# Kernel optimization log

Hardware: AMD Instinct MI355X
Metric: run time of the kernel (lower is better)

## Reference

```python
import jax, jax.numpy as jnp
import numpy as np

N, E, D, H = 50000, 600000, 128, 128
SLOPE = 0.01  # default negative_slope of F.leaky_relu / nn.LeakyReLU


def leaky(x):
    return jnp.where(x >= 0, x, SLOPE * x)


def gcn_conv(x, src, dst, W, b, n):
    """PyG GCNConv: x' = D^{-1/2}(A+I)D^{-1/2} (x W) + b, symmetric norm with self-loops."""
    h = x @ W  # [n, out]
    ones = jnp.ones(src.shape[0], h.dtype)
    deg = jax.ops.segment_sum(ones, dst, num_segments=n) + 1.0  # +1 for self-loop
    dinv = jax.lax.rsqrt(deg)  # deg >= 1 always
    norm = dinv[src] * dinv[dst]  # per-edge coefficient
    msg = h[src] * norm[:, None]  # gather + scale: [E, out]
    agg = jax.ops.segment_sum(msg, dst, num_segments=n)  # scatter-add
    agg = agg + h * (dinv * dinv)[:, None]  # self-loop term
    return agg + b


def setup_inputs() -> dict:
    key = jax.random.key(0)
    ks = jax.random.split(key, 16)
    kaiming = lambda k, fi, fo: jax.random.normal(k, (fi, fo), jnp.float32) * np.sqrt(2.0 / fi)
    return {
        "x": jax.random.normal(ks[0], (N, D), jnp.float32),
        "edge_index": jax.random.randint(ks[1], (2, E), 0, N, jnp.int64 if jax.config.jax_enable_x64 else jnp.int32),
        "gen_data": jax.random.normal(ks[2], (N, H), jnp.float32),
        "Wc1": kaiming(ks[3], D, H), "bc1": jnp.zeros((H,), jnp.float32),
        "Wc2": kaiming(ks[4], H, H), "bc2": jnp.zeros((H,), jnp.float32),
        "Wm1": kaiming(ks[5], H, H), "bm1": jnp.zeros((H,), jnp.float32),
        "Wm2": kaiming(ks[6], H, H), "bm2": jnp.zeros((H,), jnp.float32),
        "Wp1": kaiming(ks[7], H, H), "bp1": jnp.zeros((H,), jnp.float32),
        "Wp2": kaiming(ks[8], H, H), "bp2": jnp.zeros((H,), jnp.float32),
    }


def reference(x, edge_index, gen_data, Wc1, bc1, Wc2, bc2, Wm1, bm1, Wm2, bm2, Wp1, bp1, Wp2, bp2):
    src, dst = edge_index[0], edge_index[1]
    lambd = 0.5
    # GraphEncoder4Link
    h = leaky(gcn_conv(x, src, dst, Wc1, bc1, N))
    h = leaky(gcn_conv(h, src, dst, Wc2, bc2, N) + h)
    h = leaky((leaky(h @ Wm1 + bm1) @ Wm2 + bm2) + h)
    # lambd interpolation with gen_data
    out = lambd * h + (1.0 - lambd) * gen_data
    # proj MLP
    out = leaky(leaky(out @ Wp1 + bp1) @ Wp2 + bp2)
    return out
```

## Files before the change

### kernel.cpp

```cpp
#include <hip/hip_runtime.h>
#include <cstdint>
#include <cstddef>

#define HH 128
#define SLOPE 0.01f

typedef __attribute__((ext_vector_type(8))) __bf16 bf16x8;
typedef __attribute__((ext_vector_type(8))) unsigned short ushort8v;
typedef __attribute__((ext_vector_type(4))) float f32x4;

__device__ __forceinline__ float lrelu(float x) { return x >= 0.f ? x : SLOPE * x; }
__device__ __forceinline__ unsigned short f2b(float f) {
  union { float f; unsigned u; } v; v.f = f;
  unsigned r = v.u + 0x7fffu + ((v.u >> 16) & 1u);
  return (unsigned short)(r >> 16);
}
__device__ __forceinline__ float b2f(unsigned short u) {
  union { unsigned u; float f; } v; v.u = ((unsigned)u) << 16; return v.f;
}

__device__ __forceinline__ int lofs(int r, int k) {
  return (r << 7) + ((((k >> 3) ^ r) & 15) << 3) + (k & 7);
}

#define WAVE_SYNC() asm volatile("s_waitcnt lgkmcnt(0)" ::: "memory")

__device__ __forceinline__ void gll16(const void* g, void* l) {
  __builtin_amdgcn_global_load_lds((const __attribute__((address_space(1))) void*)g,
                                   (__attribute__((address_space(3))) void*)l, 16, 0, 0);
}


__global__ __launch_bounds__(256) void count_kernel(const int* __restrict__ dst,
                                                    int* __restrict__ cnt, int nE) {
  int e = blockIdx.x * 256 + threadIdx.x;
  if (e < nE) atomicAdd(&cnt[dst[e]], 1);
}

__global__ __launch_bounds__(1024) void scan1_kernel(int* __restrict__ cnt,
                                                     int* __restrict__ rowptr,
                                                     int* __restrict__ bsum,
                                                     float* __restrict__ dinv, int n) {
  __shared__ int wsum[16];
  const int tid = threadIdx.x;
  const int lane = tid & 63, wid = tid >> 6;
  int i = blockIdx.x * 1024 + tid;
  int v = (i < n) ? cnt[i] : 0;
  int x = v;
#pragma unroll
  for (int off = 1; off < 64; off <<= 1) {
    int y = __shfl_up(x, off, 64);
    if (lane >= off) x += y;
  }
  if (lane == 63) wsum[wid] = x;
  __syncthreads();
  if (tid == 0) {
    int s = 0;
#pragma unroll
    for (int w = 0; w < 16; ++w) { int t = wsum[w]; wsum[w] = s; s += t; }
    bsum[blockIdx.x] = s;
  }
  __syncthreads();
  if (i < n) {
    rowptr[i] = wsum[wid] + x - v;
    dinv[i] = rsqrtf((float)v + 1.0f);
    cnt[i] = 0;
  }
}

__global__ __launch_bounds__(64) void scan2_kernel(int* __restrict__ bsum, int nb,
                                                   int* __restrict__ rowptr, int n, int E) {
  int lane = threadIdx.x;
  int v = (lane < nb) ? bsum[lane] : 0;
  int x = v;
#pragma unroll
  for (int off = 1; off < 64; off <<= 1) {
    int y = __shfl_up(x, off, 64);
    if (lane >= off) x += y;
  }
  if (lane < nb) bsum[lane] = x - v;
  if (lane == 0) rowptr[n] = E;
}

__global__ __launch_bounds__(1024) void scan3_kernel(int* __restrict__ rowptr,
                                                     const int* __restrict__ bsum, int n) {
  int i = blockIdx.x * 1024 + threadIdx.x;
  if (i < n) rowptr[i] += bsum[blockIdx.x];
}

__global__ __launch_bounds__(256) void fill_kernel(const int* __restrict__ src,
                                                   const int* __restrict__ dst,
                                                   const int* __restrict__ rowptr,
                                                   int* __restrict__ cursor,
                                                   const float* __restrict__ dinv,
                                                   int2* __restrict__ csr, int nE) {
  int e = blockIdx.x * 256 + threadIdx.x;
  if (e >= nE) return;
  int d = dst[e], s = src[e];
  int pos = rowptr[d] + atomicAdd(&cursor[d], 1);
  int2 ent;
  ent.x = s;
  ent.y = __float_as_int(dinv[s] * dinv[d]);
  csr[pos] = ent;
}

__global__ __launch_bounds__(256) void pack_kernel(const float* W0, const float* W1,
                                                   const float* W2, const float* W3,
                                                   const float* W4, const float* W5,
                                                   unsigned short* __restrict__ out) {
  const float* Ws[6] = {W0, W1, W2, W3, W4, W5};
  const float* W = Ws[blockIdx.y];
  int f = blockIdx.x * 256 + threadIdx.x;
  int j = f & 7, L = (f >> 3) & 63, c = (f >> 9) & 7, t = f >> 12;
  int k = t * 32 + (L >> 4) * 8 + j;
  int n = c * 16 + (L & 15);
  out[(size_t)blockIdx.y * 16384 + f] = f2b(W[k * HH + n]);
}


__device__ __forceinline__ void mfma_ldsW(const bf16x8 af[4],
                                          const unsigned short* __restrict__ Wl,
                                          int lane, f32x4 acc[8]) {
#pragma unroll
  for (int c = 0; c < 8; ++c) acc[c] = (f32x4){0.f, 0.f, 0.f, 0.f};
#pragma unroll
  for (int t = 0; t < 4; ++t) {
    bf16x8 wf[8];
#pragma unroll
    for (int c = 0; c < 8; ++c) wf[c] = *(const bf16x8*)&Wl[(t * 8 + c) * 512 + lane * 8];
#pragma unroll
    for (int c = 0; c < 8; ++c)
      acc[c] = __builtin_amdgcn_mfma_f32_16x16x32_bf16(af[t], wf[c], acc[c], 0, 0, 0);
  }
}

__device__ __forceinline__ void lds_afrags16(const unsigned short* __restrict__ Tl,
                                             int m, int quad, bf16x8 af[4]) {
#pragma unroll
  for (int t = 0; t < 4; ++t)
    af[t] = *(const bf16x8*)&Tl[lofs(m, t * 32 + quad * 8)];
}


__global__ __launch_bounds__(256, 1) void gemm_conv(const float* __restrict__ A,
                                                    const unsigned short* __restrict__ Wp,
                                                    unsigned short* __restrict__ out, int nrows) {
  __shared__ __align__(16) unsigned short Wl[16384];
  const int tid = threadIdx.x;
  const int lane = tid & 63, wave = tid >> 6;
  const int row0 = blockIdx.x * 64 + wave * 16;
  const int m = lane & 15, quad = lane >> 4;

#pragma unroll
  for (int i = 0; i < 8; ++i)
    gll16((const uint4*)Wp + i * 256 + tid, (uint4*)Wl + i * 256 + wave * 64);

  const int gr = row0 + m;
  const bool rok = gr < nrows;
  const float* Arow = A + (size_t)gr * HH;
  bf16x8 af[4];
#pragma unroll
  for (int t = 0; t < 4; ++t) {
    const int k = t * 32 + quad * 8;
    float4 lo = make_float4(0.f, 0.f, 0.f, 0.f), hi = lo;
    if (rok) {
      lo = *(const float4*)(Arow + k);
      hi = *(const float4*)(Arow + k + 4);
    }
    union { ushort8v u; bf16x8 b; } cv;
    cv.u[0] = f2b(lo.x); cv.u[1] = f2b(lo.y); cv.u[2] = f2b(lo.z); cv.u[3] = f2b(lo.w);
    cv.u[4] = f2b(hi.x); cv.u[5] = f2b(hi.y); cv.u[6] = f2b(hi.z); cv.u[7] = f2b(hi.w);
    af[t] = cv.b;
  }

  __syncthreads();

  f32x4 acc[8];
  mfma_ldsW(af, Wl, lane, acc);

#pragma unroll
  for (int c = 0; c < 8; ++c) {
    int col = c * 16 + m;
#pragma unroll
    for (int g = 0; g < 4; ++g) {
      int row = row0 + quad * 4 + g;
      if (row < nrows) out[(size_t)row * HH + col] = f2b(acc[c][g]);
    }
  }
}


template <int RES, int OUTBF>
__global__ __launch_bounds__(256) void agg_kernel(const unsigned short* __restrict__ h,
                                                  const int* __restrict__ rowptr,
                                                  const int2* __restrict__ csr,
                                                  const float* __restrict__ dinv,
                                                  const float* __restrict__ bias,
                                                  const float* __restrict__ res,
                                                  void* __restrict__ outv, int n) {
  int node = blockIdx.x * 4 + (threadIdx.x >> 6);
  if (node >= n) return;
  int lane = threadIdx.x & 63;
  int c = lane << 1;
  int j = rowptr[node], end = rowptr[node + 1];
  float ax = 0.f, ay = 0.f;
  for (; j + 8 <= end; j += 8) {
    int2 e[8];
    ushort2 r[8];
#pragma unroll
    for (int q = 0; q < 8; ++q) e[q] = csr[j + q];
#pragma unroll
    for (int q = 0; q < 8; ++q) r[q] = *(const ushort2*)(h + (size_t)e[q].x * HH + c);
#pragma unroll
    for (int q = 0; q < 8; ++q) {
      float nv = __int_as_float(e[q].y);
      ax = fmaf(b2f(r[q].x), nv, ax); ay = fmaf(b2f(r[q].y), nv, ay);
    }
  }
  for (; j + 2 <= end; j += 2) {
    int2 e0 = csr[j], e1 = csr[j + 1];
    ushort2 r0 = *(const ushort2*)(h + (size_t)e0.x * HH + c);
    ushort2 r1 = *(const ushort2*)(h + (size_t)e1.x * HH + c);
    float n0 = __int_as_float(e0.y), n1 = __int_as_float(e1.y);
    ax = fmaf(b2f(r0.x), n0, ax); ay = fmaf(b2f(r0.y), n0, ay);
    ax = fmaf(b2f(r1.x), n1, ax); ay = fmaf(b2f(r1.y), n1, ay);
  }
  if (j < end) {
    int2 e0 = csr[j];
    float n0 = __int_as_float(e0.y);
    ushort2 r0 = *(const ushort2*)(h + (size_t)e0.x * HH + c);
    ax = fmaf(b2f(r0.x), n0, ax); ay = fmaf(b2f(r0.y), n0, ay);
  }
  float di = dinv[node], d2 = di * di;
  ushort2 hs = *(const ushort2*)(h + (size_t)node * HH + c);
  float2 b = *(const float2*)(bias + c);
  float ox = ax + b2f(hs.x) * d2 + b.x;
  float oy = ay + b2f(hs.y) * d2 + b.y;
  if (RES) {
    float2 r = *(const float2*)(res + (size_t)node * HH + c);
    ox += r.x; oy += r.y;
  }
  ox = lrelu(ox); oy = lrelu(oy);
  if (OUTBF) {
    ushort2 o; o.x = f2b(ox); o.y = f2b(oy);
    *(ushort2*)((unsigned short*)outv + (size_t)node * HH + c) = o;
  } else {
    *(float2*)((float*)outv + (size_t)node * HH + c) = make_float2(ox, oy);
  }
}


__global__ __launch_bounds__(256, 1) void fusedMLP(const unsigned short* __restrict__ f2bf,
                                                   const unsigned short* __restrict__ Wm1p,
                                                   const unsigned short* __restrict__ Wm2p,
                                                   const unsigned short* __restrict__ Wp1p,
                                                   const unsigned short* __restrict__ Wp2p,
                                                   const float* __restrict__ bm1,
                                                   const float* __restrict__ bm2,
                                                   const float* __restrict__ bp1,
                                                   const float* __restrict__ bp2,
                                                   const float* __restrict__ gen,
                                                   float* __restrict__ out, int n) {
  __shared__ __align__(16) unsigned short Wl[16384];
  __shared__ __align__(16) unsigned short Ta[4][16 * HH];
  __shared__ __align__(16) unsigned short Tb[4][16 * HH];
  __shared__ __align__(16) float Bi[4][4 * HH];
  const int tid = threadIdx.x;
  const int lane = tid & 63, wave = tid >> 6;
  const int row0 = blockIdx.x * 64 + wave * 16;
  const int m = lane & 15, quad = lane >> 4;
  unsigned short* TA = Ta[wave];
  unsigned short* TB = Tb[wave];
  float* BI = Bi[wave];

#pragma unroll
  for (int i = 0; i < 8; ++i)
    gll16((const uint4*)Wm1p + i * 256 + tid, (uint4*)Wl + i * 256 + wave * 64);

#pragma unroll
  for (int i = 0; i < 4; ++i) {
    int idx = i * 64 + lane;
    int r = idx >> 4, k = (idx & 15) << 3;
    int gr = row0 + r;
    ushort8v v = {0, 0, 0, 0, 0, 0, 0, 0};
    if (gr < n) v = *(const ushort8v*)(f2bf + (size_t)gr * HH + k);
    *(ushort8v*)&TA[lofs(r, k)] = v;
  }

  ushort4 genb[8];
#pragma unroll
  for (int i = 0; i < 8; ++i) {
    int idx = i * 64 + lane;
    int r = idx >> 5, c4 = (idx & 31) << 2;
    int gr = row0 + r;
    float4 v = make_float4(0.f, 0.f, 0.f, 0.f);
    if (gr < n) v = *(const float4*)(gen + (size_t)gr * HH + c4);
    genb[i].x = f2b(v.x); genb[i].y = f2b(v.y); genb[i].z = f2b(v.z); genb[i].w = f2b(v.w);
  }

  {
    const float* b01 = (lane < 32) ? bm1 : bm2;
    const float* b23 = (lane < 32) ? bp1 : bp2;
    int col = (lane & 31) << 2;
    float4 v0 = *(const float4*)(b01 + col);
    float4 v1 = *(const float4*)(b23 + col);
    *(float4*)&BI[lane * 4] = v0;
    *(float4*)&BI[256 + lane * 4] = v1;
  }

  __syncthreads();

  bf16x8 af[4];
  f32x4 acc[8];
  float bv[8];

#pragma unroll
  for (int cc = 0; cc < 8; ++cc) bv[cc] = BI[cc * 16 + m];
  lds_afrags16(TA, m, quad, af);
  mfma_ldsW(af, Wl, lane, acc);
#pragma unroll
  for (int cc = 0; cc < 8; ++cc) {
    int col = cc * 16 + m;
#pragma unroll
    for (int g = 0; g < 4; ++g)
      TB[lofs(quad * 4 + g, col)] = f2b(lrelu(acc[cc][g] + bv[cc]));
  }
  __syncthreads();

#pragma unroll
  for (int i = 0; i < 8; ++i)
    gll16((const uint4*)Wm2p + i * 256 + tid, (uint4*)Wl + i * 256 + wave * 64);
#pragma unroll
  for (int cc = 0; cc < 8; ++cc) bv[cc] = BI[128 + cc * 16 + m];
  lds_afrags16(TB, m, quad, af);
  WAVE_SYNC();
#pragma unroll
  for (int i = 0; i < 8; ++i) {
    int idx = i * 64 + lane;
    int r = idx >> 5, c4 = (idx & 31) << 2;
    *(ushort4*)&TB[lofs(r, c4)] = genb[i];
  }
  __syncthreads();

  mfma_ldsW(af, Wl, lane, acc);
#pragma unroll
  for (int cc = 0; cc < 8; ++cc) {
    int col = cc * 16 + m;
#pragma unroll
    for (int g = 0; g < 4; ++g) {
      int lr = quad * 4 + g;
      float f2v = b2f(TA[lofs(lr, col)]);
      float v = lrelu(acc[cc][g] + bv[cc] + f2v);
      float gv = b2f(TB[lofs(lr, col)]);
      TA[lofs(lr, col)] = f2b(0.5f * (v + gv));
    }
  }
  __syncthreads();

#pragma unroll
  for (int i = 0; i < 8; ++i)
    gll16((const uint4*)Wp1p + i * 256 + tid, (uint4*)Wl + i * 256 + wave * 64);
#pragma unroll
  for (int cc = 0; cc < 8; ++cc) bv[cc] = BI[256 + cc * 16 + m];
  lds_afrags16(TA, m, quad, af);
  __syncthreads();

  mfma_ldsW(af, Wl, lane, acc);
#pragma unroll
  for (int cc = 0; cc < 8; ++cc) {
    int col = cc * 16 + m;
#pragma unroll
    for (int g = 0; g < 4; ++g)
      TB[lofs(quad * 4 + g, col)] = f2b(lrelu(acc[cc][g] + bv[cc]));
  }
  __syncthreads();

#pragma unroll
  for (int i = 0; i < 8; ++i)
    gll16((const uint4*)Wp2p + i * 256 + tid, (uint4*)Wl + i * 256 + wave * 64);
#pragma unroll
  for (int cc = 0; cc < 8; ++cc) bv[cc] = BI[384 + cc * 16 + m];
  lds_afrags16(TB, m, quad, af);
  __syncthreads();

  mfma_ldsW(af, Wl, lane, acc);
#pragma unroll
  for (int cc = 0; cc < 8; ++cc) {
    int col = cc * 16 + m;
#pragma unroll
    for (int g = 0; g < 4; ++g) {
      int row = row0 + quad * 4 + g;
      if (row < n) out[(size_t)row * HH + col] = lrelu(acc[cc][g] + bv[cc]);
    }
  }
}


extern "C" void kernel_launch(void* const* d_in, const int* in_sizes, int n_in,
                              void* d_out, int out_size, void* d_ws, size_t ws_size,
                              hipStream_t stream) {
  const float* x   = (const float*)d_in[0];
  const int* ei    = (const int*)d_in[1];
  const float* gen = (const float*)d_in[2];
  const float* Wc1 = (const float*)d_in[3];
  const float* bc1 = (const float*)d_in[4];
  const float* Wc2 = (const float*)d_in[5];
  const float* bc2 = (const float*)d_in[6];
  const float* Wm1 = (const float*)d_in[7];
  const float* bm1 = (const float*)d_in[8];
  const float* Wm2 = (const float*)d_in[9];
  const float* bm2 = (const float*)d_in[10];
  const float* Wp1 = (const float*)d_in[11];
  const float* bp1 = (const float*)d_in[12];
  const float* Wp2 = (const float*)d_in[13];
  const float* bp2 = (const float*)d_in[14];

  const int N = in_sizes[0] / HH;
  const int E = in_sizes[1] / 2;
  const int* src = ei;
  const int* dst = ei + E;

  char* ws = (char*)d_ws;
  size_t off = 0;
  auto alloc = [&](size_t bytes) { void* p = ws + off; off += (bytes + 255) & ~(size_t)255; return p; };
  float* dinv            = (float*)alloc((size_t)N * 4);
  int*   rowptr          = (int*)  alloc((size_t)(N + 1) * 4);
  int*   cursor          = (int*)  alloc((size_t)N * 4);
  int*   bsum            = (int*)  alloc((size_t)64 * 4);
  int2*  csr             = (int2*) alloc((size_t)E * 8);
  unsigned short* h_bf   = (unsigned short*)alloc((size_t)N * HH * 2);
  unsigned short* t2_bf  = (unsigned short*)alloc((size_t)N * HH * 2);
  unsigned short* f2_bf  = (unsigned short*)alloc((size_t)N * HH * 2);
  float* f1_f32          = (float*)alloc((size_t)N * HH * 4);
  unsigned short* packed = (unsigned short*)alloc((size_t)6 * 16384 * 2);
  float* fOut = (float*)d_out;

  const int cblocks = (N + 63) / 64;
  const int eblocks = (E + 255) / 256;
  const int ablocks = (N + 3) / 4;
  const int sblocks = (N + 1023) / 1024;

  pack_kernel<<<dim3(64, 6), 256, 0, stream>>>(Wc1, Wc2, Wm1, Wm2, Wp1, Wp2, packed);

  hipMemsetAsync(cursor, 0, (size_t)N * 4, stream);
  count_kernel<<<eblocks, 256, 0, stream>>>(dst, cursor, E);
  scan1_kernel<<<sblocks, 1024, 0, stream>>>(cursor, rowptr, bsum, dinv, N);
  scan2_kernel<<<1, 64, 0, stream>>>(bsum, sblocks, rowptr, N, E);
  scan3_kernel<<<sblocks, 1024, 0, stream>>>(rowptr, bsum, N);
  fill_kernel<<<eblocks, 256, 0, stream>>>(src, dst, rowptr, cursor, dinv, csr, E);

  gemm_conv<<<cblocks, 256, 0, stream>>>(x, packed + 0 * 16384, h_bf, N);
  agg_kernel<0, 0><<<ablocks, 256, 0, stream>>>(h_bf, rowptr, csr, dinv, bc1, nullptr, f1_f32, N);
  gemm_conv<<<cblocks, 256, 0, stream>>>(f1_f32, packed + 1 * 16384, t2_bf, N);
  agg_kernel<1, 1><<<ablocks, 256, 0, stream>>>(t2_bf, rowptr, csr, dinv, bc2, f1_f32, f2_bf, N);
  fusedMLP<<<cblocks, 256, 0, stream>>>(f2_bf,
                                        packed + 2 * 16384, packed + 3 * 16384,
                                        packed + 4 * 16384, packed + 5 * 16384,
                                        bm1, bm2, bp1, bp2, gen, fOut, N);
}
```

Baseline: 291.3 us.

## Reuse atomic rank for CSR fill and split aggregation across half-waves

The count kernel now stores each edge's atomicAdd return value as its rank, so the fill kernel computes positions without a second round of atomics and the scan no longer resets counters. The aggregation kernel splits each wave into two halves, each handling alternate edges with 8-byte vector loads of four bf16 columns, then combines the halves with a cross-lane shuffle. This is meant to cut atomic contention in CSR construction and raise memory-level parallelism in the gather. In exchange it adds an E-sized rank buffer write and read, and half the lanes sit idle during the epilogue.

Measured after the change: 277.5 us. -4.8%, faster.

```diff
diff --git a/kernel.cpp b/kernel.cpp
--- a/kernel.cpp
+++ b/kernel.cpp
@@ -32,9 +32,10 @@
 
 
 __global__ __launch_bounds__(256) void count_kernel(const int* __restrict__ dst,
-                                                    int* __restrict__ cnt, int nE) {
+                                                    int* __restrict__ cnt,
+                                                    int* __restrict__ rank, int nE) {
   int e = blockIdx.x * 256 + threadIdx.x;
-  if (e < nE) atomicAdd(&cnt[dst[e]], 1);
+  if (e < nE) rank[e] = atomicAdd(&cnt[dst[e]], 1);
 }
 
 __global__ __launch_bounds__(1024) void scan1_kernel(int* __restrict__ cnt,
@@ -64,7 +65,6 @@
   if (i < n) {
     rowptr[i] = wsum[wid] + x - v;
     dinv[i] = rsqrtf((float)v + 1.0f);
-    cnt[i] = 0;
   }
 }
 
@@ -91,13 +91,13 @@
 __global__ __launch_bounds__(256) void fill_kernel(const int* __restrict__ src,
                                                    const int* __restrict__ dst,
                                                    const int* __restrict__ rowptr,
-                                                   int* __restrict__ cursor,
+                                                   const int* __restrict__ rank,
                                                    const float* __restrict__ dinv,
                                                    int2* __restrict__ csr, int nE) {
   int e = blockIdx.x * 256 + threadIdx.x;
   if (e >= nE) return;
   int d = dst[e], s = src[e];
-  int pos = rowptr[d] + atomicAdd(&cursor[d], 1);
+  int pos = rowptr[d] + rank[e];
   int2 ent;
   ent.x = s;
   ent.y = __float_as_int(dinv[s] * dinv[d]);
@@ -200,52 +200,67 @@
                                                   void* __restrict__ outv, int n) {
   int node = blockIdx.x * 4 + (threadIdx.x >> 6);
   if (node >= n) return;
-  int lane = threadIdx.x & 63;
-  int c = lane << 1;
-  int j = rowptr[node], end = rowptr[node + 1];
-  float ax = 0.f, ay = 0.f;
+  const int lane = threadIdx.x & 63;
+  const int p = lane >> 5;
+  const int c4 = (lane & 31) << 2;
+  int j = rowptr[node];
+  const int end = rowptr[node + 1];
+  float a0 = 0.f, a1 = 0.f, a2 = 0.f, a3 = 0.f;
+
   for (; j + 8 <= end; j += 8) {
-    int2 e[8];
-    ushort2 r[8];
-#pragma unroll
-    for (int q = 0; q < 8; ++q) e[q] = csr[j + q];
-#pragma unroll
-    for (int q = 0; q < 8; ++q) r[q] = *(const ushort2*)(h + (size_t)e[q].x * HH + c);
-#pragma unroll
-    for (int q = 0; q < 8; ++q) {
+    int2 e[4];
+    ushort4 r[4];
+#pragma unroll
+    for (int q = 0; q < 4; ++q) e[q] = csr[j + 2 * q + p];
+#pragma unroll
+    for (int q = 0; q < 4; ++q) r[q] = *(const ushort4*)(h + (size_t)e[q].x * HH + c4);
+#pragma unroll
+    for (int q = 0; q < 4; ++q) {
       float nv = __int_as_float(e[q].y);
-      ax = fmaf(b2f(r[q].x), nv, ax); ay = fmaf(b2f(r[q].y), nv, ay);
+      a0 = fmaf(b2f(r[q].x), nv, a0); a1 = fmaf(b2f(r[q].y), nv, a1);
+      a2 = fmaf(b2f(r[q].z), nv, a2); a3 = fmaf(b2f(r[q].w), nv, a3);
     }
   }
   for (; j + 2 <= end; j += 2) {
-    int2 e0 = csr[j], e1 = csr[j + 1];
-    ushort2 r0 = *(const ushort2*)(h + (size_t)e0.x * HH + c);
-    ushort2 r1 = *(const ushort2*)(h + (size_t)e1.x * HH + c);
-    float n0 = __int_as_float(e0.y), n1 = __int_as_float(e1.y);
-    ax = fmaf(b2f(r0.x), n0, ax); ay = fmaf(b2f(r0.y), n0, ay);
-    ax = fmaf(b2f(r1.x), n1, ax); ay = fmaf(b2f(r1.y), n1, ay);
-  }
-  if (j < end) {
-    int2 e0 = csr[j];
-    float n0 = __int_as_float(e0.y);
-    ushort2 r0 = *(const ushort2*)(h + (size_t)e0.x * HH + c);
-    ax = fmaf(b2f(r0.x), n0, ax); ay = fmaf(b2f(r0.y), n0, ay);
-  }
-  float di = dinv[node], d2 = di * di;
-  ushort2 hs = *(const ushort2*)(h + (size_t)node * HH + c);
-  float2 b = *(const float2*)(bias + c);
-  float ox = ax + b2f(hs.x) * d2 + b.x;
-  float oy = ay + b2f(hs.y) * d2 + b.y;
-  if (RES) {
-    float2 r = *(const float2*)(res + (size_t)node * HH + c);
-    ox += r.x; oy += r.y;
-  }
-  ox = lrelu(ox); oy = lrelu(oy);
-  if (OUTBF) {
-    ushort2 o; o.x = f2b(ox); o.y = f2b(oy);
-    *(ushort2*)((unsigned short*)outv + (size_t)node * HH + c) = o;
-  } else {
-    *(float2*)((float*)outv + (size_t)node * HH + c) = make_float2(ox, oy);
+    int2 e = csr[j + p];
+    ushort4 r = *(const ushort4*)(h + (size_t)e.x * HH + c4);
+    float nv = __int_as_float(e.y);
+    a0 = fmaf(b2f(r.x), nv, a0); a1 = fmaf(b2f(r.y), nv, a1);
+    a2 = fmaf(b2f(r.z), nv, a2); a3 = fmaf(b2f(r.w), nv, a3);
+  }
+  if (j < end && p == 0) {
+    int2 e = csr[j];
+    ushort4 r = *(const ushort4*)(h + (size_t)e.x * HH + c4);
+    float nv = __int_as_float(e.y);
+    a0 = fmaf(b2f(r.x), nv, a0); a1 = fmaf(b2f(r.y), nv, a1);
+    a2 = fmaf(b2f(r.z), nv, a2); a3 = fmaf(b2f(r.w), nv, a3);
+  }
+
+  a0 += __shfl_xor(a0, 32);
+  a1 += __shfl_xor(a1, 32);
+  a2 += __shfl_xor(a2, 32);
+  a3 += __shfl_xor(a3, 32);
+
+  if (p == 0) {
+    float di = dinv[node], d2 = di * di;
+    ushort4 hs = *(const ushort4*)(h + (size_t)node * HH + c4);
+    float4 b = *(const float4*)(bias + c4);
+    float o0 = a0 + b2f(hs.x) * d2 + b.x;
+    float o1 = a1 + b2f(hs.y) * d2 + b.y;
+    float o2 = a2 + b2f(hs.z) * d2 + b.z;
+    float o3 = a3 + b2f(hs.w) * d2 + b.w;
+    if (RES) {
+      float4 r = *(const float4*)(res + (size_t)node * HH + c4);
+      o0 += r.x; o1 += r.y; o2 += r.z; o3 += r.w;
+    }
+    o0 = lrelu(o0); o1 = lrelu(o1); o2 = lrelu(o2); o3 = lrelu(o3);
+    if (OUTBF) {
+      ushort4 o;
+      o.x = f2b(o0); o.y = f2b(o1); o.z = f2b(o2); o.w = f2b(o3);
+      *(ushort4*)((unsigned short*)outv + (size_t)node * HH + c4) = o;
+    } else {
+      *(float4*)((float*)outv + (size_t)node * HH + c4) = make_float4(o0, o1, o2, o3);
+    }
   }
 }
 
@@ -425,8 +440,9 @@
   auto alloc = [&](size_t bytes) { void* p = ws + off; off += (bytes + 255) & ~(size_t)255; return p; };
   float* dinv            = (float*)alloc((size_t)N * 4);
   int*   rowptr          = (int*)  alloc((size_t)(N + 1) * 4);
-  int*   cursor          = (int*)  alloc((size_t)N * 4);
+  int*   cnt             = (int*)  alloc((size_t)N * 4);
   int*   bsum            = (int*)  alloc((size_t)64 * 4);
+  int*   rank            = (int*)  alloc((size_t)E * 4);
   int2*  csr             = (int2*) alloc((size_t)E * 8);
   unsigned short* h_bf   = (unsigned short*)alloc((size_t)N * HH * 2);
   unsigned short* t2_bf  = (unsigned short*)alloc((size_t)N * HH * 2);
@@ -442,12 +458,12 @@
 
   pack_kernel<<<dim3(64, 6), 256, 0, stream>>>(Wc1, Wc2, Wm1, Wm2, Wp1, Wp2, packed);
 
-  hipMemsetAsync(cursor, 0, (size_t)N * 4, stream);
-  count_kernel<<<eblocks, 256, 0, stream>>>(dst, cursor, E);
-  scan1_kernel<<<sblocks, 1024, 0, stream>>>(cursor, rowptr, bsum, dinv, N);
+  hipMemsetAsync(cnt, 0, (size_t)N * 4, stream);
+  count_kernel<<<eblocks, 256, 0, stream>>>(dst, cnt, rank, E);
+  scan1_kernel<<<sblocks, 1024, 0, stream>>>(cnt, rowptr, bsum, dinv, N);
   scan2_kernel<<<1, 64, 0, stream>>>(bsum, sblocks, rowptr, N, E);
   scan3_kernel<<<sblocks, 1024, 0, stream>>>(rowptr, bsum, N);
-  fill_kernel<<<eblocks, 256, 0, stream>>>(src, dst, rowptr, cursor, dinv, csr, E);
+  fill_kernel<<<eblocks, 256, 0, stream>>>(src, dst, rowptr, rank, dinv, csr, E);
 
   gemm_conv<<<cblocks, 256, 0, stream>>>(x, packed + 0 * 16384, h_bf, N);
   agg_kernel<0, 0><<<ablocks, 256, 0, stream>>>(h_bf, rowptr, csr, dinv, bc1, nullptr, f1_f32, N);
```
